# Performance work log

Hardware: AMD Instinct MI355X
Metric: run time of the kernel (lower is better)

The kernel has to match this reference:

```python
import jax, jax.numpy as jnp
import numpy as np

D = 256  # input_dim


def setup_inputs() -> dict:
    key = jax.random.key(0)
    ks = jax.random.split(key, 10)
    s = 1.0 / np.sqrt(D)  # torch Linear init scale (uniform bound)
    desc0 = jax.random.normal(ks[0], (4, 4096, D), dtype=jnp.float32)
    desc1 = jax.random.normal(ks[1], (4, 4096, D), dtype=jnp.float32)
    def lin(kw, kb):
        W = jax.random.uniform(kw, (D, D), jnp.float32, -s, s)
        b = jax.random.uniform(kb, (D,), jnp.float32, -s, s)
        return W, b
    Wq, bq = lin(ks[2], ks[3])
    Wk, bk = lin(ks[4], ks[5])
    Wv, bv = lin(ks[6], ks[7])
    Wo, bo = lin(ks[8], ks[9])
    return {"desc0": desc0, "desc1": desc1,
            "Wq": Wq, "bq": bq, "Wk": Wk, "bk": bk,
            "Wv": Wv, "bv": bv, "Wo": Wo, "bo": bo}


def reference(desc0, desc1, Wq, bq, Wk, bk, Wv, bv, Wo, bo):
    # torch Linear: y = x @ W.T + b
    q = desc0 @ Wq.T + bq                      # [B, N0, D]
    k = desc1 @ Wk.T + bk                      # [B, N1, D]
    v = desc1 @ Wv.T + bv                      # [B, N1, D]
    scale = 1.0 / jnp.sqrt(jnp.asarray(q.shape[-1], q.dtype))
    attn = jnp.einsum('bqd,bkd->bqk', q, k) * scale  # [B, N0, N1]
    weights = jax.nn.softmax(attn, axis=-1)
    out = jnp.einsum('bqk,bkd->bqd', weights, v)     # [B, N0, D]
    return out @ Wo.T + bo
```

## Files before the change

### kernel.cpp

```cpp
#include <hip/hip_runtime.h>


typedef __attribute__((ext_vector_type(8))) __bf16 bf16x8;
typedef __attribute__((ext_vector_type(4))) float f32x4;
typedef __attribute__((ext_vector_type(16))) float f32x16;
typedef __attribute__((ext_vector_type(4))) unsigned int u32x4;
typedef __attribute__((ext_vector_type(2))) unsigned int u32x2;
typedef __attribute__((ext_vector_type(4))) unsigned short us16x4;

__device__ __forceinline__ unsigned short f2bf(float f) {
  unsigned u = __builtin_bit_cast(unsigned, f);
  u += 0x7FFFu + ((u >> 16) & 1u);
  return (unsigned short)(u >> 16);
}
__device__ __forceinline__ unsigned pk2(float a, float b) {
  return (unsigned)f2bf(a) | ((unsigned)f2bf(b) << 16);
}
__device__ __forceinline__ unsigned cvtpk(float lo, float hi) {
  unsigned r;
  asm("v_cvt_pk_bf16_f32 %0, %1, %2" : "=v"(r) : "v"(lo), "v"(hi));
  return r;
}
__device__ __forceinline__ float bf2f(unsigned short s) {
  return __builtin_bit_cast(float, ((unsigned)s) << 16);
}
__device__ __forceinline__ int swz4(int r) { return (r ^ (r >> 2)) & 3; }
__device__ __forceinline__ bf16x8 ldbf16(const void* p) {
  return __builtin_bit_cast(bf16x8, *(const u32x4*)p);
}
__device__ __forceinline__ f32x4 mfma16(bf16x8 a, bf16x8 b, f32x4 c) {
  return __builtin_amdgcn_mfma_f32_16x16x32_bf16(a, b, c, 0, 0, 0);
}
__device__ __forceinline__ f32x16 mfma32(bf16x8 a, bf16x8 b, f32x16 c) {
  return __builtin_amdgcn_mfma_f32_32x32x16_bf16(a, b, c, 0, 0, 0);
}
__device__ __forceinline__ void gld16(void* lds, const void* gsrc) {
  __builtin_amdgcn_global_load_lds(
      (const __attribute__((address_space(1))) unsigned int*)gsrc,
      (__attribute__((address_space(3))) unsigned int*)lds, 16, 0, 0);
}

__global__ __launch_bounds__(256, 4) void qkv_k(
    const float* __restrict__ desc0, const float* __restrict__ desc1,
    const float* __restrict__ Wq, const float* __restrict__ bq,
    const float* __restrict__ Wk, const float* __restrict__ bk,
    const float* __restrict__ Wv, const float* __restrict__ bv,
    unsigned short* __restrict__ qout, unsigned short* __restrict__ kout,
    unsigned short* __restrict__ vout) {
  __shared__ __align__(16) unsigned short Al[2][64 * 32];
  __shared__ __align__(16) unsigned short W1l[2][64 * 32];
  __shared__ __align__(16) unsigned short W2l[2][64 * 32];
  __shared__ float b1l[64], b2l[64];
  const int tid = threadIdx.x;
  const int w = tid >> 6, l = tid & 63, g = l >> 4, c = l & 15;
  const int bid = blockIdx.x;
  const bool iskv = bid >= 1024;
  const int bb = iskv ? bid - 1024 : bid;
  const int mt = bb & 255, nq = bb >> 8;
  const int row0 = mt * 64, n0 = nq * 64;
  const float* A = iskv ? desc1 : desc0;
  const float* W1 = iskv ? Wk : Wq;
  const float qs = iskv ? 1.f : 0.09016844f;
  if (tid < 64) {
    b1l[tid] = (iskv ? bk : bq)[n0 + tid] * qs;
    if (iskv) b2l[tid] = bv[n0 + tid];
  }

  const int sr = tid >> 2, seg = tid & 3;
  const int ssw = swz4(sr);

#define CONV8(dst, X, Y)                                                              \
  {                                                                                   \
    u32x4 _v;                                                                         \
    _v[0] = cvtpk((X).x, (X).y); _v[1] = cvtpk((X).z, (X).w);                         \
    _v[2] = cvtpk((Y).x, (Y).y); _v[3] = cvtpk((Y).z, (Y).w);                         \
    *(u32x4*)(dst) = _v;                                                              \
  }
#define CONV8S(dst, X, Y, S)                                                          \
  {                                                                                   \
    u32x4 _v;                                                                         \
    _v[0] = cvtpk((X).x * (S), (X).y * (S)); _v[1] = cvtpk((X).z * (S), (X).w * (S)); \
    _v[2] = cvtpk((Y).x * (S), (Y).y * (S)); _v[3] = cvtpk((Y).z * (S), (Y).w * (S)); \
    *(u32x4*)(dst) = _v;                                                              \
  }

  {
    const float* ap = A + (size_t)(row0 + sr) * 256 + seg * 8;
    float4 ax = *(const float4*)ap, ay = *(const float4*)(ap + 4);
    CONV8(&Al[0][sr * 32 + ((seg ^ ssw) << 3)], ax, ay);
    const float* wp = W1 + (size_t)(n0 + sr) * 256 + seg * 8;
    float4 wx = *(const float4*)wp, wy = *(const float4*)(wp + 4);
    CONV8S(&W1l[0][sr * 32 + ((seg ^ ssw) << 3)], wx, wy, qs);
    if (iskv) {
      const float* wp2 = Wv + (size_t)(n0 + sr) * 256 + seg * 8;
      float4 w2x = *(const float4*)(wp2), w2y = *(const float4*)(wp2 + 4);
      CONV8(&W2l[0][sr * 32 + ((seg ^ ssw) << 3)], w2x, w2y);
    }
  }
  __syncthreads();

  f32x4 acc1[4], acc2[4];
#pragma unroll
  for (int jt = 0; jt < 4; ++jt) {
    acc1[jt] = (f32x4){0.f, 0.f, 0.f, 0.f};
    acc2[jt] = (f32x4){0.f, 0.f, 0.f, 0.f};
  }

#pragma unroll 1
  for (int ch = 0; ch < 8; ++ch) {
    const int cur = ch & 1;
    const bool pre = (ch + 1 < 8);
    float4 ax, ay, wx, wy, w2x, w2y;
    if (pre) {
      const int ko = (ch + 1) * 32 + seg * 8;
      const float* ap = A + (size_t)(row0 + sr) * 256 + ko;
      ax = *(const float4*)ap; ay = *(const float4*)(ap + 4);
      const float* wp = W1 + (size_t)(n0 + sr) * 256 + ko;
      wx = *(const float4*)wp; wy = *(const float4*)(wp + 4);
      if (iskv) {
        const float* wp2 = Wv + (size_t)(n0 + sr) * 256 + ko;
        w2x = *(const float4*)wp2; w2y = *(const float4*)(wp2 + 4);
      }
    }
    const int ra = w * 16 + c;
    bf16x8 af = ldbf16(&Al[cur][ra * 32 + ((g ^ swz4(ra)) << 3)]);
#pragma unroll
    for (int jt = 0; jt < 4; ++jt) {
      const int j = jt * 16 + c;
      bf16x8 w1f = ldbf16(&W1l[cur][j * 32 + ((g ^ swz4(j)) << 3)]);
      acc1[jt] = mfma16(af, w1f, acc1[jt]);
    }
    if (iskv) {
#pragma unroll
      for (int jt = 0; jt < 4; ++jt) {
        const int j = jt * 16 + c;
        bf16x8 w2f = ldbf16(&W2l[cur][j * 32 + ((g ^ swz4(j)) << 3)]);
        acc2[jt] = mfma16(af, w2f, acc2[jt]);
      }
    }
    if (pre) {
      CONV8(&Al[1 - cur][sr * 32 + ((seg ^ ssw) << 3)], ax, ay);
      CONV8S(&W1l[1 - cur][sr * 32 + ((seg ^ ssw) << 3)], wx, wy, qs);
      if (iskv) CONV8(&W2l[1 - cur][sr * 32 + ((seg ^ ssw) << 3)], w2x, w2y);
    }
    __syncthreads();
  }
#undef CONV8
#undef CONV8S

  unsigned short* o1 = iskv ? kout : qout;
  const int rloc = w * 16 + (g << 2);
#pragma unroll
  for (int jt = 0; jt < 4; ++jt) {
    const int col = n0 + jt * 16 + c;
    const float bvv = b1l[jt * 16 + c];
#pragma unroll
    for (int r = 0; r < 4; ++r)
      o1[(size_t)(row0 + rloc + r) * 256 + col] = f2bf(acc1[jt][r] + bvv);
  }
  if (iskv) {
    const int n = row0 + rloc;
    const int b = n >> 12, nl = n & 4095;
#pragma unroll
    for (int jt = 0; jt < 4; ++jt) {
      const int col = n0 + jt * 16 + c;
      const float bvv = b2l[jt * 16 + c];
      u32x2 pkv;
      pkv[0] = cvtpk(acc2[jt][0] + bvv, acc2[jt][1] + bvv);
      pkv[1] = cvtpk(acc2[jt][2] + bvv, acc2[jt][3] + bvv);
      *(u32x2*)(vout + (size_t)b * 1048576 + (size_t)(nl >> 6) * 16384 + col * 64 + (nl & 63)) = pkv;
    }
  }
}

template <int IN_MODE>
__global__ __launch_bounds__(256, 4) void projo_k(const unsigned short* __restrict__ Ain,
                                                  const float* __restrict__ W,
                                                  const float* __restrict__ bias,
                                                  float* __restrict__ Cout,
                                                  const float* __restrict__ lwA) {
  __shared__ __align__(16) unsigned short Al[2][64 * 32];
  __shared__ __align__(16) unsigned short Wl[2][64 * 32];
  __shared__ float biasl[64];
  const int tid = threadIdx.x;
  const int w = tid >> 6, l = tid & 63, g = l >> 4, c = l & 15;
  const int mt = blockIdx.x & 255, nq = blockIdx.x >> 8;
  const int row0 = mt * 64, n0 = nq * 64;
  if (tid < 64) biasl[tid] = bias[n0 + tid];

  const int sr = tid >> 2, seg = tid & 3;
  const int ssw = swz4(sr);

  float ainv;
  {
    const int grow = row0 + sr;
    float lt = lwA[grow];
    if (IN_MODE == 2) lt += lwA[16384 + grow];
    ainv = 1.f / lt;
  }

#define ACONV(dst, M0, M1)                                                          \
  {                                                                                 \
    u32x4 _v;                                                                       \
    _Pragma("unroll") for (int i = 0; i < 4; ++i) {                                 \
      float _lo = bf2f((unsigned short)((M0)[i] & 0xFFFF));                         \
      float _hi = bf2f((unsigned short)((M0)[i] >> 16));                            \
      if (IN_MODE == 2) {                                                           \
        _lo += bf2f((unsigned short)((M1)[i] & 0xFFFF));                            \
        _hi += bf2f((unsigned short)((M1)[i] >> 16));                               \
      }                                                                             \
      _v[i] = cvtpk(_lo * ainv, _hi * ainv);                                        \
    }                                                                               \
    *(u32x4*)(dst) = _v;                                                            \
  }

  {
    const unsigned short* ap = Ain + (size_t)(row0 + sr) * 256 + seg * 8;
    u32x4 a0 = *(const u32x4*)ap;
    u32x4 a1 = (IN_MODE == 2) ? *(const u32x4*)(ap + 4194304) : a0;
    ACONV(&Al[0][sr * 32 + ((seg ^ ssw) << 3)], a0, a1);
    const float* wp = W + (size_t)(n0 + sr) * 256 + seg * 8;
    float4 x = *(const float4*)wp, y = *(const float4*)(wp + 4);
    u32x4 v; v[0] = cvtpk(x.x, x.y); v[1] = cvtpk(x.z, x.w);
    v[2] = cvtpk(y.x, y.y); v[3] = cvtpk(y.z, y.w);
    *(u32x4*)&Wl[0][sr * 32 + ((seg ^ ssw) << 3)] = v;
  }
  __syncthreads();

  f32x4 acc[4];
#pragma unroll
  for (int jt = 0; jt < 4; ++jt) acc[jt] = (f32x4){0.f, 0.f, 0.f, 0.f};

#pragma unroll 1
  for (int ch = 0; ch < 8; ++ch) {
    const int cur = ch & 1;
    const bool pre = (ch + 1 < 8);
    float4 wx, wy; u32x4 abv, abv2;
    if (pre) {
      const int ko = (ch + 1) * 32 + seg * 8;
      const unsigned short* ap = Ain + (size_t)(row0 + sr) * 256 + ko;
      abv = *(const u32x4*)ap;
      if (IN_MODE == 2) abv2 = *(const u32x4*)(ap + 4194304);
      const float* wp = W + (size_t)(n0 + sr) * 256 + ko;
      wx = *(const float4*)wp; wy = *(const float4*)(wp + 4);
    }
    const int ra = w * 16 + c;
    bf16x8 af = ldbf16(&Al[cur][ra * 32 + ((g ^ swz4(ra)) << 3)]);
#pragma unroll
    for (int jt = 0; jt < 4; ++jt) {
      const int j = jt * 16 + c;
      bf16x8 bfr = ldbf16(&Wl[cur][j * 32 + ((g ^ swz4(j)) << 3)]);
      acc[jt] = mfma16(af, bfr, acc[jt]);
    }
    if (pre) {
      ACONV(&Al[1 - cur][sr * 32 + ((seg ^ ssw) << 3)], abv, abv2);
      u32x4 vw; vw[0] = cvtpk(wx.x, wx.y); vw[1] = cvtpk(wx.z, wx.w);
      vw[2] = cvtpk(wy.x, wy.y); vw[3] = cvtpk(wy.z, wy.w);
      *(u32x4*)&Wl[1 - cur][sr * 32 + ((seg ^ ssw) << 3)] = vw;
    }
    __syncthreads();
  }
#undef ACONV

#pragma unroll
  for (int jt = 0; jt < 4; ++jt) {
    const int col = n0 + jt * 16 + c;
    const float bv = biasl[jt * 16 + c];
    const int rloc = w * 16 + (g << 2);
#pragma unroll
    for (int r = 0; r < 4; ++r)
      Cout[(size_t)(row0 + rloc + r) * 256 + col] = acc[jt][r] + bv;
  }
}

template <int NS>
__global__ __launch_bounds__(512, 2) void attn_k(const unsigned short* __restrict__ qg,
                                                 const unsigned short* __restrict__ kg,
                                                 const unsigned short* __restrict__ vg,
                                                 unsigned short* __restrict__ part,
                                                 float* __restrict__ lw) {
  __shared__ __align__(16) unsigned char smem[148480];
  const int tid = threadIdx.x, w = tid >> 6, l = tid & 63;
  const int l31 = l & 31, h5 = l >> 5;
  const int qt = w >> 1, hf = w & 1;
  const int dh = w >> 1, qh = w & 1;
  const int bid = blockIdx.x;
  const int b4 = bid & 3;
  const int s = (NS == 2) ? ((bid >> 2) & 1) : 0;
  const int qtl = (NS == 2) ? (bid >> 3) : (bid >> 2);
  const int q0 = qtl * 128;
  const int NT = (NS == 2) ? 32 : 64;

  const unsigned short* kb = kg + (size_t)b4 * 1048576 + (size_t)s * 524288;
  const unsigned short* vb = vg + (size_t)b4 * 1048576 + (size_t)s * 32 * 16384;

  bf16x8 qf[16];
  {
    const unsigned short* qp = qg + ((size_t)b4 * 4096 + q0 + qt * 32 + l31) * 256;
#pragma unroll
    for (int kst = 0; kst < 16; ++kst) qf[kst] = ldbf16(qp + kst * 16 + h5 * 8);
  }

  f32x16 o[4];
#pragma unroll
  for (int d = 0; d < 4; ++d)
#pragma unroll
    for (int r = 0; r < 16; ++r) o[d][r] = 0.f;
  float l_run = 0.f;

  int goffK[4], goffV[4];
#pragma unroll
  for (int i = 0; i < 4; ++i) {
    const int sl = i * 512 + tid;
    const int kk = sl >> 5, ch = sl & 31;
    goffK[i] = kk * 256 + ((ch ^ (kk & 31)) << 3);
    const int r = sl >> 4, p16 = sl & 15;
    const int x = p16 ^ (r & 15);
    goffV[i] = (2 * r + (x >> 3)) * 64 + ((x & 7) << 3);
  }
#define STAGE(buf, t1)                                                                   \
  {                                                                                      \
    const unsigned short* _ks = kb + (size_t)(t1) * 16384;                               \
    const unsigned short* _vs = vb + (size_t)(t1) * 16384;                               \
    _Pragma("unroll") for (int i = 0; i < 4; ++i)                                        \
        gld16(smem + (buf) * 32768 + i * 8192 + w * 1024, _ks + goffK[i]);               \
    _Pragma("unroll") for (int i = 0; i < 4; ++i)                                        \
        gld16(smem + 65536 + (buf) * 32768 + i * 8192 + w * 1024, _vs + goffV[i]);       \
  }

  STAGE(0, 0);
  __syncthreads();

  unsigned char* Pq = smem + 131072 + qt * 4096;
  const int kkr = hf * 32 + l31;

#pragma unroll 1
  for (int t = 0; t < NT; ++t) {
    const int cur = t & 1;
    if (t + 1 < NT) STAGE(1 - cur, t + 1);

    const unsigned char* Kc = smem + cur * 32768 + kkr * 512;
    f32x16 sa, sb;
#pragma unroll
    for (int r = 0; r < 16; ++r) { sa[r] = 0.f; sb[r] = 0.f; }
    __builtin_amdgcn_s_setprio(1);
#pragma unroll
    for (int kst = 0; kst < 16; ++kst) {
      bf16x8 kf = ldbf16(Kc + (((kst * 2 + h5) ^ l31) << 4));
      if (kst & 1) sb = mfma32(kf, qf[kst], sb);
      else         sa = mfma32(kf, qf[kst], sa);
    }
    __builtin_amdgcn_s_setprio(0);

    const unsigned char* Vc = smem + 65536 + cur * 32768;
    bf16x8 va[8];
#pragma unroll
    for (int dd = 0; dd < 2; ++dd) {
      const int dm = dh * 64 + dd * 32 + l31;
      const int rr = dm >> 1;
      const unsigned char* Vr = Vc + rr * 256;
      const int xb = (dm & 1) * 8;
#pragma unroll
      for (int kst = 0; kst < 4; ++kst)
        va[dd * 4 + kst] = ldbf16(Vr + (((xb + kst * 2 + h5) ^ (rr & 15)) << 4));
    }

    float p[16];
#pragma unroll
    for (int r = 0; r < 16; ++r) p[r] = exp2f(sa[r] + sb[r]);
    float ls = ((p[0] + p[1]) + (p[2] + p[3])) + ((p[4] + p[5]) + (p[6] + p[7])) +
               (((p[8] + p[9]) + (p[10] + p[11])) + ((p[12] + p[13]) + (p[14] + p[15])));
    l_run += ls;

    unsigned u[8];
#pragma unroll
    for (int i = 0; i < 8; ++i) u[i] = cvtpk(p[2 * i], p[2 * i + 1]);
#pragma unroll
    for (int j = 0; j < 4; ++j) {
      u32x2 dv; dv[0] = u[2 * j]; dv[1] = u[2 * j + 1];
      *(u32x2*)(Pq + l31 * 128 + (((j + 4 * hf) ^ (l31 & 7)) << 4) + h5 * 8) = dv;
    }

    asm volatile("s_waitcnt lgkmcnt(0)\n\ts_barrier" ::: "memory");
    __builtin_amdgcn_sched_barrier(0);

    __builtin_amdgcn_s_setprio(1);
#pragma unroll
    for (int qq = 0; qq < 2; ++qq) {
      const unsigned char* Pr = smem + 131072 + (qh * 2 + qq) * 4096;
      bf16x8 pb[4];
#pragma unroll
      for (int kst = 0; kst < 4; ++kst)
        pb[kst] = ldbf16(Pr + l31 * 128 + (((kst * 2 + h5) ^ (l31 & 7)) << 4));
#pragma unroll
      for (int dd = 0; dd < 2; ++dd)
#pragma unroll
        for (int kst = 0; kst < 4; ++kst)
          o[dd * 2 + qq] = mfma32(va[dd * 4 + kst], pb[kst], o[dd * 2 + qq]);
    }
    __builtin_amdgcn_s_setprio(0);

    __syncthreads();
  }
#undef STAGE

  l_run += __shfl_xor(l_run, 32);

  float* Lb = (float*)(smem + 147456);
  if (l < 32) Lb[(qt * 2 + hf) * 32 + l31] = l_run;
  __syncthreads();

  unsigned char* T = smem + w * 16384;
#pragma unroll
  for (int dd = 0; dd < 2; ++dd)
#pragma unroll
    for (int qq = 0; qq < 2; ++qq)
#pragma unroll
      for (int rg = 0; rg < 4; ++rg) {
        f32x4 wv;
        wv[0] = o[dd * 2 + qq][4 * rg + 0]; wv[1] = o[dd * 2 + qq][4 * rg + 1];
        wv[2] = o[dd * 2 + qq][4 * rg + 2]; wv[3] = o[dd * 2 + qq][4 * rg + 3];
        const int qloc = qq * 32 + l31;
        const int c16 = dd * 8 + rg * 2 + h5;
        *(f32x4*)(T + qloc * 256 + ((c16 ^ (qloc & 15)) << 4)) = wv;
      }
  asm volatile("s_waitcnt lgkmcnt(0)" ::: "memory");
  __builtin_amdgcn_sched_barrier(0);
  {
    const int qloc = l;
    f32x4 rv[16];
#pragma unroll
    for (int c16 = 0; c16 < 16; ++c16)
      rv[c16] = *(const f32x4*)(T + qloc * 256 + ((c16 ^ (qloc & 15)) << 4));
    unsigned short* op = part + (size_t)s * 4194304 +
                         ((size_t)b4 * 4096 + q0 + qh * 64 + qloc) * 256 + dh * 64;
#pragma unroll
    for (int i = 0; i < 8; ++i) {
      u32x4 ov;
      ov[0] = cvtpk(rv[2 * i][0], rv[2 * i][1]);
      ov[1] = cvtpk(rv[2 * i][2], rv[2 * i][3]);
      ov[2] = cvtpk(rv[2 * i + 1][0], rv[2 * i + 1][1]);
      ov[3] = cvtpk(rv[2 * i + 1][2], rv[2 * i + 1][3]);
      *(u32x4*)(op + i * 8) = ov;
    }
  }
  if (hf == 0 && l < 32) {
    const float lt = Lb[(qt * 2) * 32 + l31] + Lb[(qt * 2 + 1) * 32 + l31];
    lw[(size_t)s * 16384 + (size_t)b4 * 4096 + q0 + qt * 32 + l31] = lt;
  }
}

extern "C" void kernel_launch(void* const* d_in, const int* in_sizes, int n_in,
                              void* d_out, int out_size, void* d_ws, size_t ws_size,
                              hipStream_t stream) {
  (void)in_sizes; (void)n_in; (void)out_size;
  const float* desc0 = (const float*)d_in[0];
  const float* desc1 = (const float*)d_in[1];
  const float* Wq = (const float*)d_in[2];
  const float* bq = (const float*)d_in[3];
  const float* Wk = (const float*)d_in[4];
  const float* bk = (const float*)d_in[5];
  const float* Wv = (const float*)d_in[6];
  const float* bv = (const float*)d_in[7];
  const float* Wo = (const float*)d_in[8];
  const float* bo = (const float*)d_in[9];

  unsigned char* ws = (unsigned char*)d_ws;
  unsigned short* qw = (unsigned short*)(ws);
  unsigned short* kw = (unsigned short*)(ws + 8388608);
  unsigned short* vw = (unsigned short*)(ws + 16777216);
  unsigned short* part = (unsigned short*)(ws + 25165824);
  float* lwp = (float*)(ws + 41943040);

  const bool two = (ws_size >= 42008576ull);

  qkv_k<<<2048, 256, 0, stream>>>(desc0, desc1, Wq, bq, Wk, bk, Wv, bv, qw, kw, vw);
  if (two) {
    attn_k<2><<<256, 512, 0, stream>>>(qw, kw, vw, part, lwp);
    projo_k<2><<<1024, 256, 0, stream>>>(part, Wo, bo, (float*)d_out, lwp);
  } else {
    lwp = (float*)(ws + 33554432);
    attn_k<1><<<128, 512, 0, stream>>>(qw, kw, vw, part, lwp);
    projo_k<3><<<1024, 256, 0, stream>>>(part, Wo, bo, (float*)d_out, lwp);
  }
}
```

Before: 118.8 us.

## Pre-convert weights to bf16 once and stage them via direct global-to-LDS loads

Adds a small kernel that converts Wq (with the softmax scale folded in), Wk, Wv and Wo to bf16 into workspace once per call. The QKV and output projection kernels then load bf16 weight tiles straight into LDS with global_load_lds, instead of loading fp32, converting in registers and storing to LDS on every block. This removes redundant per-block conversion work and halves weight read traffic, and frees registers. The cost is an extra kernel launch and a larger workspace requirement, which changes the threshold that selects the two-split path.

```diff
diff --git a/kernel.cpp b/kernel.cpp
--- a/kernel.cpp
+++ b/kernel.cpp
@@ -13,9 +13,6 @@
   u += 0x7FFFu + ((u >> 16) & 1u);
   return (unsigned short)(u >> 16);
 }
-__device__ __forceinline__ unsigned pk2(float a, float b) {
-  return (unsigned)f2bf(a) | ((unsigned)f2bf(b) << 16);
-}
 __device__ __forceinline__ unsigned cvtpk(float lo, float hi) {
   unsigned r;
   asm("v_cvt_pk_bf16_f32 %0, %1, %2" : "=v"(r) : "v"(lo), "v"(hi));
@@ -40,11 +37,28 @@
       (__attribute__((address_space(3))) unsigned int*)lds, 16, 0, 0);
 }
 
+__global__ __launch_bounds__(256, 8) void wconv_k(const float* __restrict__ w0,
+                                                  const float* __restrict__ w1,
+                                                  const float* __restrict__ w2,
+                                                  const float* __restrict__ w3,
+                                                  unsigned short* __restrict__ out) {
+  const int b = blockIdx.x, t = threadIdx.x;
+  const int wi = b >> 5;
+  const float* src = wi == 0 ? w0 : wi == 1 ? w1 : wi == 2 ? w2 : w3;
+  const float sc = (wi == 0) ? 0.09016844f : 1.f;
+  const int idx = ((b & 31) * 256 + t) * 8;
+  float4 x = *(const float4*)(src + idx), y = *(const float4*)(src + idx + 4);
+  u32x4 v;
+  v[0] = cvtpk(x.x * sc, x.y * sc); v[1] = cvtpk(x.z * sc, x.w * sc);
+  v[2] = cvtpk(y.x * sc, y.y * sc); v[3] = cvtpk(y.z * sc, y.w * sc);
+  *(u32x4*)(out + (size_t)wi * 65536 + idx) = v;
+}
+
 __global__ __launch_bounds__(256, 4) void qkv_k(
     const float* __restrict__ desc0, const float* __restrict__ desc1,
-    const float* __restrict__ Wq, const float* __restrict__ bq,
-    const float* __restrict__ Wk, const float* __restrict__ bk,
-    const float* __restrict__ Wv, const float* __restrict__ bv,
+    const unsigned short* __restrict__ wbf,
+    const float* __restrict__ bq, const float* __restrict__ bk,
+    const float* __restrict__ bv,
     unsigned short* __restrict__ qout, unsigned short* __restrict__ kout,
     unsigned short* __restrict__ vout) {
   __shared__ __align__(16) unsigned short Al[2][64 * 32];
@@ -59,15 +73,16 @@
   const int mt = bb & 255, nq = bb >> 8;
   const int row0 = mt * 64, n0 = nq * 64;
   const float* A = iskv ? desc1 : desc0;
-  const float* W1 = iskv ? Wk : Wq;
-  const float qs = iskv ? 1.f : 0.09016844f;
+  const unsigned short* wb1 = wbf + (iskv ? 65536 : 0);
+  const unsigned short* wb2 = wbf + 2 * 65536;
   if (tid < 64) {
-    b1l[tid] = (iskv ? bk : bq)[n0 + tid] * qs;
+    b1l[tid] = iskv ? bk[n0 + tid] : bq[n0 + tid] * 0.09016844f;
     if (iskv) b2l[tid] = bv[n0 + tid];
   }
 
   const int sr = tid >> 2, seg = tid & 3;
   const int ssw = swz4(sr);
+  const int wsrc = (size_t)0 + ((seg ^ ssw) << 3);
 
 #define CONV8(dst, X, Y)                                                              \
   {                                                                                   \
@@ -76,26 +91,20 @@
     _v[2] = cvtpk((Y).x, (Y).y); _v[3] = cvtpk((Y).z, (Y).w);                         \
     *(u32x4*)(dst) = _v;                                                              \
   }
-#define CONV8S(dst, X, Y, S)                                                          \
+#define STAGEW(buf, ch1)                                                              \
   {                                                                                   \
-    u32x4 _v;                                                                         \
-    _v[0] = cvtpk((X).x * (S), (X).y * (S)); _v[1] = cvtpk((X).z * (S), (X).w * (S)); \
-    _v[2] = cvtpk((Y).x * (S), (Y).y * (S)); _v[3] = cvtpk((Y).z * (S), (Y).w * (S)); \
-    *(u32x4*)(dst) = _v;                                                              \
+    gld16((unsigned char*)W1l[buf] + tid * 16,                                        \
+          wb1 + (size_t)(n0 + sr) * 256 + (ch1) * 32 + wsrc);                         \
+    if (iskv)                                                                         \
+      gld16((unsigned char*)W2l[buf] + tid * 16,                                      \
+            wb2 + (size_t)(n0 + sr) * 256 + (ch1) * 32 + wsrc);                       \
   }
 
   {
+    STAGEW(0, 0);
     const float* ap = A + (size_t)(row0 + sr) * 256 + seg * 8;
     float4 ax = *(const float4*)ap, ay = *(const float4*)(ap + 4);
     CONV8(&Al[0][sr * 32 + ((seg ^ ssw) << 3)], ax, ay);
-    const float* wp = W1 + (size_t)(n0 + sr) * 256 + seg * 8;
-    float4 wx = *(const float4*)wp, wy = *(const float4*)(wp + 4);
-    CONV8S(&W1l[0][sr * 32 + ((seg ^ ssw) << 3)], wx, wy, qs);
-    if (iskv) {
-      const float* wp2 = Wv + (size_t)(n0 + sr) * 256 + seg * 8;
-      float4 w2x = *(const float4*)(wp2), w2y = *(const float4*)(wp2 + 4);
-      CONV8(&W2l[0][sr * 32 + ((seg ^ ssw) << 3)], w2x, w2y);
-    }
   }
   __syncthreads();
 
@@ -110,17 +119,12 @@
   for (int ch = 0; ch < 8; ++ch) {
     const int cur = ch & 1;
     const bool pre = (ch + 1 < 8);
-    float4 ax, ay, wx, wy, w2x, w2y;
+    float4 ax, ay;
     if (pre) {
       const int ko = (ch + 1) * 32 + seg * 8;
       const float* ap = A + (size_t)(row0 + sr) * 256 + ko;
       ax = *(const float4*)ap; ay = *(const float4*)(ap + 4);
-      const float* wp = W1 + (size_t)(n0 + sr) * 256 + ko;
-      wx = *(const float4*)wp; wy = *(const float4*)(wp + 4);
-      if (iskv) {
-        const float* wp2 = Wv + (size_t)(n0 + sr) * 256 + ko;
-        w2x = *(const float4*)wp2; w2y = *(const float4*)(wp2 + 4);
-      }
+      STAGEW(1 - cur, ch + 1);
     }
     const int ra = w * 16 + c;
     bf16x8 af = ldbf16(&Al[cur][ra * 32 + ((g ^ swz4(ra)) << 3)]);
@@ -138,15 +142,11 @@
         acc2[jt] = mfma16(af, w2f, acc2[jt]);
       }
     }
-    if (pre) {
-      CONV8(&Al[1 - cur][sr * 32 + ((seg ^ ssw) << 3)], ax, ay);
-      CONV8S(&W1l[1 - cur][sr * 32 + ((seg ^ ssw) << 3)], wx, wy, qs);
-      if (iskv) CONV8(&W2l[1 - cur][sr * 32 + ((seg ^ ssw) << 3)], w2x, w2y);
-    }
+    if (pre) CONV8(&Al[1 - cur][sr * 32 + ((seg ^ ssw) << 3)], ax, ay);
     __syncthreads();
   }
 #undef CONV8
-#undef CONV8S
+#undef STAGEW
 
   unsigned short* o1 = iskv ? kout : qout;
   const int rloc = w * 16 + (g << 2);
@@ -175,7 +175,7 @@
 
 template <int IN_MODE>
 __global__ __launch_bounds__(256, 4) void projo_k(const unsigned short* __restrict__ Ain,
-                                                  const float* __restrict__ W,
+                                                  const unsigned short* __restrict__ Wb,
                                                   const float* __restrict__ bias,
                                                   float* __restrict__ Cout,
                                                   const float* __restrict__ lwA) {
@@ -190,6 +190,7 @@
 
   const int sr = tid >> 2, seg = tid & 3;
   const int ssw = swz4(sr);
+  const int wsrc = (seg ^ ssw) << 3;
 
   float ainv;
   {
@@ -213,17 +214,16 @@
     }                                                                               \
     *(u32x4*)(dst) = _v;                                                            \
   }
+#define STAGEW(buf, ch1)                                                            \
+  gld16((unsigned char*)Wl[buf] + tid * 16,                                         \
+        Wb + (size_t)(n0 + sr) * 256 + (ch1) * 32 + wsrc);
 
   {
+    STAGEW(0, 0);
     const unsigned short* ap = Ain + (size_t)(row0 + sr) * 256 + seg * 8;
     u32x4 a0 = *(const u32x4*)ap;
     u32x4 a1 = (IN_MODE == 2) ? *(const u32x4*)(ap + 4194304) : a0;
     ACONV(&Al[0][sr * 32 + ((seg ^ ssw) << 3)], a0, a1);
-    const float* wp = W + (size_t)(n0 + sr) * 256 + seg * 8;
-    float4 x = *(const float4*)wp, y = *(const float4*)(wp + 4);
-    u32x4 v; v[0] = cvtpk(x.x, x.y); v[1] = cvtpk(x.z, x.w);
-    v[2] = cvtpk(y.x, y.y); v[3] = cvtpk(y.z, y.w);
-    *(u32x4*)&Wl[0][sr * 32 + ((seg ^ ssw) << 3)] = v;
   }
   __syncthreads();
 
@@ -235,14 +235,13 @@
   for (int ch = 0; ch < 8; ++ch) {
     const int cur = ch & 1;
     const bool pre = (ch + 1 < 8);
-    float4 wx, wy; u32x4 abv, abv2;
+    u32x4 abv, abv2;
     if (pre) {
       const int ko = (ch + 1) * 32 + seg * 8;
       const unsigned short* ap = Ain + (size_t)(row0 + sr) * 256 + ko;
       abv = *(const u32x4*)ap;
       if (IN_MODE == 2) abv2 = *(const u32x4*)(ap + 4194304);
-      const float* wp = W + (size_t)(n0 + sr) * 256 + ko;
-      wx = *(const float4*)wp; wy = *(const float4*)(wp + 4);
+      STAGEW(1 - cur, ch + 1);
     }
     const int ra = w * 16 + c;
     bf16x8 af = ldbf16(&Al[cur][ra * 32 + ((g ^ swz4(ra)) << 3)]);
@@ -252,15 +251,11 @@
       bf16x8 bfr = ldbf16(&Wl[cur][j * 32 + ((g ^ swz4(j)) << 3)]);
       acc[jt] = mfma16(af, bfr, acc[jt]);
     }
-    if (pre) {
-      ACONV(&Al[1 - cur][sr * 32 + ((seg ^ ssw) << 3)], abv, abv2);
-      u32x4 vw; vw[0] = cvtpk(wx.x, wx.y); vw[1] = cvtpk(wx.z, wx.w);
-      vw[2] = cvtpk(wy.x, wy.y); vw[3] = cvtpk(wy.z, wy.w);
-      *(u32x4*)&Wl[1 - cur][sr * 32 + ((seg ^ ssw) << 3)] = vw;
-    }
+    if (pre) ACONV(&Al[1 - cur][sr * 32 + ((seg ^ ssw) << 3)], abv, abv2);
     __syncthreads();
   }
 #undef ACONV
+#undef STAGEW
 
 #pragma unroll
   for (int jt = 0; jt < 4; ++jt) {
@@ -470,17 +465,25 @@
   unsigned short* kw = (unsigned short*)(ws + 8388608);
   unsigned short* vw = (unsigned short*)(ws + 16777216);
   unsigned short* part = (unsigned short*)(ws + 25165824);
-  float* lwp = (float*)(ws + 41943040);
-
-  const bool two = (ws_size >= 42008576ull);
-
-  qkv_k<<<2048, 256, 0, stream>>>(desc0, desc1, Wq, bq, Wk, bk, Wv, bv, qw, kw, vw);
+
+  const bool two = (ws_size >= 42598400ull);
+  float* lwp;
+  unsigned short* wbf;
+  if (two) {
+    lwp = (float*)(ws + 41943040);
+    wbf = (unsigned short*)(ws + 42074112);
+  } else {
+    lwp = (float*)(ws + 33554432);
+    wbf = (unsigned short*)(ws + 33685504);
+  }
+
+  wconv_k<<<128, 256, 0, stream>>>(Wq, Wk, Wv, Wo, wbf);
+  qkv_k<<<2048, 256, 0, stream>>>(desc0, desc1, wbf, bq, bk, bv, qw, kw, vw);
   if (two) {
     attn_k<2><<<256, 512, 0, stream>>>(qw, kw, vw, part, lwp);
-    projo_k<2><<<1024, 256, 0, stream>>>(part, Wo, bo, (float*)d_out, lwp);
+    projo_k<2><<<1024, 256, 0, stream>>>(part, wbf + 3 * 65536, bo, (float*)d_out, lwp);
   } else {
-    lwp = (float*)(ws + 33554432);
     attn_k<1><<<128, 512, 0, stream>>>(qw, kw, vw, part, lwp);
-    projo_k<3><<<1024, 256, 0, stream>>>(part, Wo, bo, (float*)d_out, lwp);
-  }
-}
+    projo_k<3><<<1024, 256, 0, stream>>>(part, wbf + 3 * 65536, bo, (float*)d_out, lwp);
+  }
+}
```

Result: slower. 121.1 us (+2.0%).
